# Performance work log

Hardware: AMD Instinct MI355X
Metric: run time of the kernel (lower is better)

## Reference

```python
import jax, jax.numpy as jnp
import numpy as np

N_NODES = 10000
N_EDGES = 640000
D = 128
N_GRAPHS = 16
N_CLASSES = 10


def setup_inputs() -> dict:
    key = jax.random.key(0)
    ks = jax.random.split(key, 12)
    x = jax.random.normal(ks[0], (N_NODES, D), dtype=jnp.float32)
    edge_index = jax.random.randint(ks[1], (2, N_EDGES), 0, N_NODES, dtype=jnp.int64)
    batch_ids = jnp.sort(jax.random.randint(ks[2], (N_NODES,), 0, N_GRAPHS, dtype=jnp.int64))
    s = 1.0 / np.sqrt(D)
    W_in = jax.random.normal(ks[3], (D, D), dtype=jnp.float32) * s
    W_self = jax.random.normal(ks[4], (D, D), dtype=jnp.float32) * s
    b = jnp.zeros((D,), dtype=jnp.float32)
    W_e1 = jax.random.normal(ks[5], (2 * D, D), dtype=jnp.float32) * (1.0 / np.sqrt(2 * D))
    b_e1 = jnp.zeros((D,), dtype=jnp.float32)
    W_e2 = jax.random.normal(ks[6], (D, 1), dtype=jnp.float32) * s
    b_e2 = jnp.zeros((1,), dtype=jnp.float32)
    W_cls = jax.random.normal(ks[7], (D, N_CLASSES), dtype=jnp.float32) * s
    b_cls = jnp.zeros((N_CLASSES,), dtype=jnp.float32)
    return {"x": x, "edge_index": edge_index, "batch_ids": batch_ids,
            "W_in": W_in, "W_self": W_self, "b": b,
            "W_e1": W_e1, "b_e1": b_e1, "W_e2": W_e2, "b_e2": b_e2,
            "W_cls": W_cls, "b_cls": b_cls}


def reference(x, edge_index, batch_ids, W_in, W_self, b, W_e1, b_e1, W_e2, b_e2, W_cls, b_cls):
    src, dst = edge_index[0], edge_index[1]
    # --- gnn(data) -> (z_node, z_graph) : GCN-style message passing ---
    h = x @ W_in                                  # [N, D]
    agg = jax.ops.segment_sum(h[src], dst, num_segments=N_NODES)  # [N, D]
    z_node = jax.nn.relu(agg + x @ W_self + b)    # [N, D]
    # mean pool per graph -> z_graph [B, D]
    sums = jax.ops.segment_sum(z_node, batch_ids, num_segments=N_GRAPHS)
    counts = jax.ops.segment_sum(jnp.ones((N_NODES,), dtype=z_node.dtype), batch_ids, num_segments=N_GRAPHS)
    z_graph = sums / jnp.maximum(counts, 1.0)[:, None]
    # --- edge predictor: gather, concat, MLP ---
    edge_features = jnp.concatenate([z_node[src], z_node[dst]], axis=1)  # [E, 2D]
    pred_edge = jax.nn.relu(edge_features @ W_e1 + b_e1) @ W_e2 + b_e2   # [E, 1]
    # --- classifier ---
    pred_class = z_graph @ W_cls + b_cls          # [B, n_classes]
    return (pred_edge, pred_class)
```

## Files before the change

kernel.cpp:

```cpp
#include <hip/hip_runtime.h>

#define N_NODES   10000
#define N_EDGES   640000
#define DIM       128
#define N_GRAPHS  16
#define N_CLASSES 10

typedef unsigned int uint;
typedef unsigned short ushort;

__device__ __forceinline__ float bf2f(uint lo16) {
    return __uint_as_float(lo16 << 16);
}
__device__ __forceinline__ ushort f2bf(float f) {
    uint u = __float_as_uint(f);
    u += 0x7fffu + ((u >> 16) & 1u);
    return (ushort)(u >> 16);
}

__global__ __launch_bounds__(256) void conv_bf16(
    const float* __restrict__ x, uint* __restrict__ xb)
{
    const int idx = blockIdx.x * 256 + threadIdx.x;
    const float4 v = ((const float4*)x)[idx];
    uint lo = (uint)f2bf(v.x) | ((uint)f2bf(v.y) << 16);
    uint hi = (uint)f2bf(v.z) | ((uint)f2bf(v.w) << 16);
    ((uint2*)xb)[idx] = make_uint2(lo, hi);
}

__global__ __launch_bounds__(256) void hist_dst(
    const int* __restrict__ dst, int* __restrict__ cnt)
{
    const int base = (blockIdx.x * 256 + threadIdx.x) * 4;
    const int d0 = dst[base + 0];
    const int d1 = dst[base + 1];
    const int d2 = dst[base + 2];
    const int d3 = dst[base + 3];
    atomicAdd(&cnt[d0], 1);
    atomicAdd(&cnt[d1], 1);
    atomicAdd(&cnt[d2], 1);
    atomicAdd(&cnt[d3], 1);
}

__global__ __launch_bounds__(256) void count_nodes(
    const int* __restrict__ bid, float* __restrict__ gcnt)
{
    __shared__ int h[N_GRAPHS];
    const int t = threadIdx.x;
    if (t < N_GRAPHS) h[t] = 0;
    __syncthreads();
    for (int n = t; n < N_NODES; n += 256) atomicAdd(&h[bid[n]], 1);
    __syncthreads();
    if (t < N_GRAPHS) gcnt[t] = (float)h[t];
}

__global__ __launch_bounds__(1024) void scan_k(
    const int* __restrict__ cnt, int* __restrict__ cursor)
{
    __shared__ int s[1024];
    const int t = threadIdx.x;
    int local[10];
    int sum = 0;
    if (t < 1000) {
        for (int j = 0; j < 10; ++j) { local[j] = sum; sum += cnt[t * 10 + j]; }
    }
    s[t] = (t < 1000) ? sum : 0;
    __syncthreads();
    for (int st = 1; st < 1024; st <<= 1) {
        int v = (t >= st) ? s[t - st] : 0;
        __syncthreads();
        s[t] += v;
        __syncthreads();
    }
    if (t < 1000) {
        const int off = (t == 0) ? 0 : s[t - 1];
        for (int j = 0; j < 10; ++j) cursor[t * 10 + j] = off + local[j];
    }
}

__global__ __launch_bounds__(256) void fill_csr(
    const int* __restrict__ src, const int* __restrict__ dst,
    int* __restrict__ cursor, uint2* __restrict__ pairs)
{
    const int base = (blockIdx.x * 256 + threadIdx.x) * 4;
    const int d0 = dst[base + 0];
    const int d1 = dst[base + 1];
    const int d2 = dst[base + 2];
    const int d3 = dst[base + 3];
    const int s0 = src[base + 0];
    const int s1 = src[base + 1];
    const int s2 = src[base + 2];
    const int s3 = src[base + 3];
    const int p0 = atomicAdd(&cursor[d0], 1);
    const int p1 = atomicAdd(&cursor[d1], 1);
    const int p2 = atomicAdd(&cursor[d2], 1);
    const int p3 = atomicAdd(&cursor[d3], 1);
    pairs[p0] = make_uint2((uint)s0, (uint)(base + 0));
    pairs[p1] = make_uint2((uint)s1, (uint)(base + 1));
    pairs[p2] = make_uint2((uint)s2, (uint)(base + 2));
    pairs[p3] = make_uint2((uint)s3, (uint)(base + 3));
}

__global__ __launch_bounds__(256) void gather_xb(
    const uint* __restrict__ xb,
    const int* __restrict__ cnt, const int* __restrict__ cursor,
    const uint2* __restrict__ pairs,
    float* __restrict__ XAGG)
{
    const int n    = blockIdx.x * 4 + (threadIdx.x >> 6);
    const int lane = threadIdx.x & 63;
    const int end  = cursor[n];
    int i = end - cnt[n];

    float a0 = 0.f, b0 = 0.f, a1 = 0.f, b1 = 0.f;
    float a2 = 0.f, b2 = 0.f, a3 = 0.f, b3 = 0.f;

    for (; i + 8 <= end; i += 8) {
        const uint v0 = xb[pairs[i + 0].x * 64 + lane];
        const uint v1 = xb[pairs[i + 1].x * 64 + lane];
        const uint v2 = xb[pairs[i + 2].x * 64 + lane];
        const uint v3 = xb[pairs[i + 3].x * 64 + lane];
        const uint v4 = xb[pairs[i + 4].x * 64 + lane];
        const uint v5 = xb[pairs[i + 5].x * 64 + lane];
        const uint v6 = xb[pairs[i + 6].x * 64 + lane];
        const uint v7 = xb[pairs[i + 7].x * 64 + lane];
        a0 += bf2f(v0 & 0xffffu); b0 += bf2f(v0 >> 16);
        a1 += bf2f(v1 & 0xffffu); b1 += bf2f(v1 >> 16);
        a2 += bf2f(v2 & 0xffffu); b2 += bf2f(v2 >> 16);
        a3 += bf2f(v3 & 0xffffu); b3 += bf2f(v3 >> 16);
        a0 += bf2f(v4 & 0xffffu); b0 += bf2f(v4 >> 16);
        a1 += bf2f(v5 & 0xffffu); b1 += bf2f(v5 >> 16);
        a2 += bf2f(v6 & 0xffffu); b2 += bf2f(v6 >> 16);
        a3 += bf2f(v7 & 0xffffu); b3 += bf2f(v7 >> 16);
    }
    for (; i < end; ++i) {
        const uint v = xb[pairs[i].x * 64 + lane];
        a0 += bf2f(v & 0xffffu); b0 += bf2f(v >> 16);
    }
    float2 s;
    s.x = (a0 + a1) + (a2 + a3);
    s.y = (b0 + b1) + (b2 + b3);
    *(float2*)&XAGG[n * DIM + lane * 2] = s;
}

#define ZROWS 8
__global__ __launch_bounds__(256) void gemm_zu(
    const float* __restrict__ XAGG_in, const float* __restrict__ x,
    const float* __restrict__ W_in, const float* __restrict__ W_self,
    const float* __restrict__ b, const int* __restrict__ bid,
    const float* __restrict__ W_e1, const float* __restrict__ b_e1,
    float* __restrict__ gsum, ushort* __restrict__ U12)
{
    __shared__ float sa[ZROWS * DIM];
    __shared__ float sb[ZROWS * DIM];
    __shared__ int sbid[ZROWS];
    const int base = blockIdx.x * ZROWS;
    const int t = threadIdx.x;
    {
        const float4* ga = (const float4*)(XAGG_in + base * DIM);
        const float4* gb = (const float4*)(x + base * DIM);
        float4* la = (float4*)sa;
        float4* lb = (float4*)sb;
        for (int i = t; i < ZROWS * DIM / 4; i += 256) { la[i] = ga[i]; lb[i] = gb[i]; }
        if (t < ZROWS) sbid[t] = bid[base + t];
    }
    __syncthreads();

    const int half = t >> 7, c = t & 127;

    {
        const float* __restrict__ W = half ? W_self : W_in;
        const float4* A4 = (const float4*)(half ? sb : sa);
        float acc[ZROWS];
#pragma unroll
        for (int r = 0; r < ZROWS; ++r) acc[r] = 0.f;
        for (int k4 = 0; k4 < DIM / 4; ++k4) {
            const float w0 = W[(k4 * 4 + 0) * DIM + c];
            const float w1 = W[(k4 * 4 + 1) * DIM + c];
            const float w2 = W[(k4 * 4 + 2) * DIM + c];
            const float w3 = W[(k4 * 4 + 3) * DIM + c];
#pragma unroll
            for (int r = 0; r < ZROWS; ++r) {
                const float4 xv = A4[r * (DIM / 4) + k4];
                acc[r] = fmaf(xv.x, w0, acc[r]);
                acc[r] = fmaf(xv.y, w1, acc[r]);
                acc[r] = fmaf(xv.z, w2, acc[r]);
                acc[r] = fmaf(xv.w, w3, acc[r]);
            }
        }
        __syncthreads();
        if (half) {
#pragma unroll
            for (int r = 0; r < ZROWS; ++r) sb[r * DIM + c] = acc[r];
        }
        __syncthreads();
        if (!half) {
            const float bv = b[c];
            float run = 0.f;
            int cur = sbid[0];
#pragma unroll
            for (int r = 0; r < ZROWS; ++r) {
                const float z = fmaxf(acc[r] + sb[r * DIM + c] + bv, 0.f);
                sa[r * DIM + c] = z;
                const int g = sbid[r];
                if (g != cur) { unsafeAtomicAdd(&gsum[cur * DIM + c], run); run = 0.f; cur = g; }
                run += z;
            }
            unsafeAtomicAdd(&gsum[cur * DIM + c], run);
        }
        __syncthreads();
    }

    {
        const float* __restrict__ W = W_e1 + half * 128 * DIM;
        const float4* Z4 = (const float4*)sa;
        float acc[ZROWS];
#pragma unroll
        for (int r = 0; r < ZROWS; ++r) acc[r] = 0.f;
        for (int k4 = 0; k4 < DIM / 4; ++k4) {
            const float w0 = W[(k4 * 4 + 0) * DIM + c];
            const float w1 = W[(k4 * 4 + 1) * DIM + c];
            const float w2 = W[(k4 * 4 + 2) * DIM + c];
            const float w3 = W[(k4 * 4 + 3) * DIM + c];
#pragma unroll
            for (int r = 0; r < ZROWS; ++r) {
                const float4 xv = Z4[r * (DIM / 4) + k4];
                acc[r] = fmaf(xv.x, w0, acc[r]);
                acc[r] = fmaf(xv.y, w1, acc[r]);
                acc[r] = fmaf(xv.z, w2, acc[r]);
                acc[r] = fmaf(xv.w, w3, acc[r]);
            }
        }
        const float bv = half ? 0.f : b_e1[c];
        for (int r = 0; r < ZROWS; ++r)
            U12[(base + r) * 256 + half * 128 + c] = f2bf(acc[r] + bv);
    }
}

__device__ __forceinline__ void ch2(uint a, uint b, float wl, float wh,
                                    float& accl, float& acch)
{
    const float fl = fmaxf(__uint_as_float(a << 16) + __uint_as_float(b << 16), 0.f);
    const float fh = fmaxf(__uint_as_float(a & 0xffff0000u) + __uint_as_float(b & 0xffff0000u), 0.f);
    accl = fmaf(fl, wl, accl);
    acch = fmaf(fh, wh, acch);
}

__global__ __launch_bounds__(256) void edge_mlp4(
    const ushort* __restrict__ U12,
    const int* __restrict__ cnt, const int* __restrict__ cursor,
    const uint2* __restrict__ pairs,
    const float* __restrict__ W_e2, const float* __restrict__ b_e2,
    float* __restrict__ out)
{
    __shared__ float ws[DIM];
    const int t = threadIdx.x;
    if (t < DIM) ws[t] = W_e2[t];
    __syncthreads();

    const int l16 = t & 15;
    const int grp = t >> 4;
    const int n   = blockIdx.x * 16 + grp;

    const int end = cursor[n];
    int i = end - cnt[n];

    const uint4 u2 = *(const uint4*)(U12 + n * 256 + 128 + l16 * 8);
    const float4 w0 = ((const float4*)ws)[l16 * 2 + 0];
    const float4 w1 = ((const float4*)ws)[l16 * 2 + 1];
    const float be2 = b_e2[0];

    for (; i + 2 <= end; i += 2) {
        const uint2 pa = pairs[i];
        const uint2 pb = pairs[i + 1];
        const uint4 A = *(const uint4*)(U12 + pa.x * 256 + l16 * 8);
        const uint4 B = *(const uint4*)(U12 + pb.x * 256 + l16 * 8);
        float p0 = 0.f, p1 = 0.f, q0 = 0.f, q1 = 0.f;
        ch2(A.x, u2.x, w0.x, w0.y, p0, p1);
        ch2(A.y, u2.y, w0.z, w0.w, p0, p1);
        ch2(A.z, u2.z, w1.x, w1.y, p0, p1);
        ch2(A.w, u2.w, w1.z, w1.w, p0, p1);
        ch2(B.x, u2.x, w0.x, w0.y, q0, q1);
        ch2(B.y, u2.y, w0.z, w0.w, q0, q1);
        ch2(B.z, u2.z, w1.x, w1.y, q0, q1);
        ch2(B.w, u2.w, w1.z, w1.w, q0, q1);
        float p = p0 + p1;
        float q = q0 + q1;
#pragma unroll
        for (int off = 8; off >= 1; off >>= 1) {
            p += __shfl_xor(p, off);
            q += __shfl_xor(q, off);
        }
        if (l16 == 0) { out[pa.y] = p + be2; out[pb.y] = q + be2; }
    }
    if (i < end) {
        const uint2 pa = pairs[i];
        const uint4 A = *(const uint4*)(U12 + pa.x * 256 + l16 * 8);
        float p0 = 0.f, p1 = 0.f;
        ch2(A.x, u2.x, w0.x, w0.y, p0, p1);
        ch2(A.y, u2.y, w0.z, w0.w, p0, p1);
        ch2(A.z, u2.z, w1.x, w1.y, p0, p1);
        ch2(A.w, u2.w, w1.z, w1.w, p0, p1);
        float p = p0 + p1;
#pragma unroll
        for (int off = 8; off >= 1; off >>= 1)
            p += __shfl_xor(p, off);
        if (l16 == 0) out[pa.y] = p + be2;
    }
}

__global__ __launch_bounds__(256) void classify(
    const float* __restrict__ gsum, const float* __restrict__ gcnt,
    const float* __restrict__ W_cls, const float* __restrict__ b_cls,
    float* __restrict__ out)
{
    const int t = threadIdx.x;
    if (t >= N_GRAPHS * N_CLASSES) return;
    const int g = t / N_CLASSES;
    const int c = t % N_CLASSES;
    const float inv = 1.0f / fmaxf(gcnt[g], 1.0f);
    float acc = 0.f;
    for (int k = 0; k < DIM; ++k)
        acc += gsum[g * DIM + k] * W_cls[k * N_CLASSES + c];
    out[g * N_CLASSES + c] = acc * inv + b_cls[c];
}

extern "C" void kernel_launch(void* const* d_in, const int* in_sizes, int n_in,
                              void* d_out, int out_size, void* d_ws, size_t ws_size,
                              hipStream_t stream)
{
    const float* x      = (const float*)d_in[0];
    const int*   eidx   = (const int*)  d_in[1];
    const int*   bid    = (const int*)  d_in[2];
    const float* W_in   = (const float*)d_in[3];
    const float* W_self = (const float*)d_in[4];
    const float* b      = (const float*)d_in[5];
    const float* W_e1   = (const float*)d_in[6];
    const float* b_e1   = (const float*)d_in[7];
    const float* W_e2   = (const float*)d_in[8];
    const float* b_e2   = (const float*)d_in[9];
    const float* W_cls  = (const float*)d_in[10];
    const float* b_cls  = (const float*)d_in[11];
    float* out = (float*)d_out;

    char* ws = (char*)d_ws;
    int*    cnt    = (int*)   (ws);
    float*  gsum   = (float*) (ws + 40960);
    float*  gcnt   = (float*) (ws + 49152);
    int*    cursor = (int*)   (ws + 65536);
    uint2*  pairs  = (uint2*) (ws + 131072);
    float*  XAGG   = (float*) (ws + 131072 + 5120000);
    ushort* U12    = (ushort*)(ws + 131072 + 10240000);
    uint*   xb     = (uint*)  (ws + 131072 + 15360000);

    const int* src = eidx;
    const int* dst = eidx + N_EDGES;

    hipMemsetAsync(d_ws, 0, 65536, stream);

    conv_bf16  <<<(N_NODES * DIM / 4) / 256, 256, 0, stream>>>(x, xb);
    hist_dst   <<<N_EDGES / 1024, 256, 0, stream>>>(dst, cnt);
    count_nodes<<<1, 256, 0, stream>>>(bid, gcnt);
    scan_k     <<<1, 1024, 0, stream>>>(cnt, cursor);
    fill_csr   <<<N_EDGES / 1024, 256, 0, stream>>>(src, dst, cursor, pairs);
    gather_xb  <<<N_NODES / 4, 256, 0, stream>>>(xb, cnt, cursor, pairs, XAGG);
    gemm_zu    <<<N_NODES / ZROWS, 256, 0, stream>>>(XAGG, x, W_in, W_self, b, bid,
                                                     W_e1, b_e1, gsum, U12);
    edge_mlp4  <<<N_NODES / 16, 256, 0, stream>>>(U12, cnt, cursor, pairs, W_e2, b_e2, out);
    classify   <<<1, 256, 0, stream>>>(gsum, gcnt, W_cls, b_cls, out + N_EDGES);
}
```

Baseline: 282.4 us.

## Process edge MLP per edge in original order and shrink CSR to source-only

The edge predictor no longer walks the dst-sorted CSR. It now assigns two edges per 16-lane group in original edge order and gathers both the source and destination U12 rows directly, writing outputs with coalesced float2 stores. Because edge ids are no longer needed, the CSR array shrinks from (src, edge id) pairs to src only, which halves fill_csr writes and gather_xb index reads. In exchange, the edge kernel loses reuse of the per-destination U2 row and does one extra random gather per edge, but it gains perfect load balance and coalesced output.

New measurement: 262.1 us. 7.2% less time.

```diff
diff --git a/kernel.cpp b/kernel.cpp
--- a/kernel.cpp
+++ b/kernel.cpp
@@ -80,7 +80,7 @@
 
 __global__ __launch_bounds__(256) void fill_csr(
     const int* __restrict__ src, const int* __restrict__ dst,
-    int* __restrict__ cursor, uint2* __restrict__ pairs)
+    int* __restrict__ cursor, uint* __restrict__ srcs)
 {
     const int base = (blockIdx.x * 256 + threadIdx.x) * 4;
     const int d0 = dst[base + 0];
@@ -95,16 +95,16 @@
     const int p1 = atomicAdd(&cursor[d1], 1);
     const int p2 = atomicAdd(&cursor[d2], 1);
     const int p3 = atomicAdd(&cursor[d3], 1);
-    pairs[p0] = make_uint2((uint)s0, (uint)(base + 0));
-    pairs[p1] = make_uint2((uint)s1, (uint)(base + 1));
-    pairs[p2] = make_uint2((uint)s2, (uint)(base + 2));
-    pairs[p3] = make_uint2((uint)s3, (uint)(base + 3));
+    srcs[p0] = (uint)s0;
+    srcs[p1] = (uint)s1;
+    srcs[p2] = (uint)s2;
+    srcs[p3] = (uint)s3;
 }
 
 __global__ __launch_bounds__(256) void gather_xb(
     const uint* __restrict__ xb,
     const int* __restrict__ cnt, const int* __restrict__ cursor,
-    const uint2* __restrict__ pairs,
+    const uint* __restrict__ srcs,
     float* __restrict__ XAGG)
 {
     const int n    = blockIdx.x * 4 + (threadIdx.x >> 6);
@@ -116,14 +116,14 @@
     float a2 = 0.f, b2 = 0.f, a3 = 0.f, b3 = 0.f;
 
     for (; i + 8 <= end; i += 8) {
-        const uint v0 = xb[pairs[i + 0].x * 64 + lane];
-        const uint v1 = xb[pairs[i + 1].x * 64 + lane];
-        const uint v2 = xb[pairs[i + 2].x * 64 + lane];
-        const uint v3 = xb[pairs[i + 3].x * 64 + lane];
-        const uint v4 = xb[pairs[i + 4].x * 64 + lane];
-        const uint v5 = xb[pairs[i + 5].x * 64 + lane];
-        const uint v6 = xb[pairs[i + 6].x * 64 + lane];
-        const uint v7 = xb[pairs[i + 7].x * 64 + lane];
+        const uint v0 = xb[srcs[i + 0] * 64 + lane];
+        const uint v1 = xb[srcs[i + 1] * 64 + lane];
+        const uint v2 = xb[srcs[i + 2] * 64 + lane];
+        const uint v3 = xb[srcs[i + 3] * 64 + lane];
+        const uint v4 = xb[srcs[i + 4] * 64 + lane];
+        const uint v5 = xb[srcs[i + 5] * 64 + lane];
+        const uint v6 = xb[srcs[i + 6] * 64 + lane];
+        const uint v7 = xb[srcs[i + 7] * 64 + lane];
         a0 += bf2f(v0 & 0xffffu); b0 += bf2f(v0 >> 16);
         a1 += bf2f(v1 & 0xffffu); b1 += bf2f(v1 >> 16);
         a2 += bf2f(v2 & 0xffffu); b2 += bf2f(v2 >> 16);
@@ -134,7 +134,7 @@
         a3 += bf2f(v7 & 0xffffu); b3 += bf2f(v7 >> 16);
     }
     for (; i < end; ++i) {
-        const uint v = xb[pairs[i].x * 64 + lane];
+        const uint v = xb[srcs[i] * 64 + lane];
         a0 += bf2f(v & 0xffffu); b0 += bf2f(v >> 16);
     }
     float2 s;
@@ -246,10 +246,9 @@
     acch = fmaf(fh, wh, acch);
 }
 
-__global__ __launch_bounds__(256) void edge_mlp4(
+__global__ __launch_bounds__(256) void edge_mlp5(
     const ushort* __restrict__ U12,
-    const int* __restrict__ cnt, const int* __restrict__ cursor,
-    const uint2* __restrict__ pairs,
+    const int* __restrict__ src, const int* __restrict__ dst,
     const float* __restrict__ W_e2, const float* __restrict__ b_e2,
     float* __restrict__ out)
 {
@@ -260,52 +259,40 @@
 
     const int l16 = t & 15;
     const int grp = t >> 4;
-    const int n   = blockIdx.x * 16 + grp;
-
-    const int end = cursor[n];
-    int i = end - cnt[n];
-
-    const uint4 u2 = *(const uint4*)(U12 + n * 256 + 128 + l16 * 8);
+    const int e0  = blockIdx.x * 32 + grp * 2;
+    const int e1  = e0 + 1;
+
+    const int s0 = src[e0], d0 = dst[e0];
+    const int s1 = src[e1], d1 = dst[e1];
+
+    const uint4 A0 = *(const uint4*)(U12 + s0 * 256 + l16 * 8);
+    const uint4 B0 = *(const uint4*)(U12 + d0 * 256 + 128 + l16 * 8);
+    const uint4 A1 = *(const uint4*)(U12 + s1 * 256 + l16 * 8);
+    const uint4 B1 = *(const uint4*)(U12 + d1 * 256 + 128 + l16 * 8);
     const float4 w0 = ((const float4*)ws)[l16 * 2 + 0];
     const float4 w1 = ((const float4*)ws)[l16 * 2 + 1];
-    const float be2 = b_e2[0];
-
-    for (; i + 2 <= end; i += 2) {
-        const uint2 pa = pairs[i];
-        const uint2 pb = pairs[i + 1];
-        const uint4 A = *(const uint4*)(U12 + pa.x * 256 + l16 * 8);
-        const uint4 B = *(const uint4*)(U12 + pb.x * 256 + l16 * 8);
-        float p0 = 0.f, p1 = 0.f, q0 = 0.f, q1 = 0.f;
-        ch2(A.x, u2.x, w0.x, w0.y, p0, p1);
-        ch2(A.y, u2.y, w0.z, w0.w, p0, p1);
-        ch2(A.z, u2.z, w1.x, w1.y, p0, p1);
-        ch2(A.w, u2.w, w1.z, w1.w, p0, p1);
-        ch2(B.x, u2.x, w0.x, w0.y, q0, q1);
-        ch2(B.y, u2.y, w0.z, w0.w, q0, q1);
-        ch2(B.z, u2.z, w1.x, w1.y, q0, q1);
-        ch2(B.w, u2.w, w1.z, w1.w, q0, q1);
-        float p = p0 + p1;
-        float q = q0 + q1;
-#pragma unroll
-        for (int off = 8; off >= 1; off >>= 1) {
-            p += __shfl_xor(p, off);
-            q += __shfl_xor(q, off);
-        }
-        if (l16 == 0) { out[pa.y] = p + be2; out[pb.y] = q + be2; }
-    }
-    if (i < end) {
-        const uint2 pa = pairs[i];
-        const uint4 A = *(const uint4*)(U12 + pa.x * 256 + l16 * 8);
-        float p0 = 0.f, p1 = 0.f;
-        ch2(A.x, u2.x, w0.x, w0.y, p0, p1);
-        ch2(A.y, u2.y, w0.z, w0.w, p0, p1);
-        ch2(A.z, u2.z, w1.x, w1.y, p0, p1);
-        ch2(A.w, u2.w, w1.z, w1.w, p0, p1);
-        float p = p0 + p1;
-#pragma unroll
-        for (int off = 8; off >= 1; off >>= 1)
-            p += __shfl_xor(p, off);
-        if (l16 == 0) out[pa.y] = p + be2;
+
+    float p0 = 0.f, p1 = 0.f, q0 = 0.f, q1 = 0.f;
+    ch2(A0.x, B0.x, w0.x, w0.y, p0, p1);
+    ch2(A0.y, B0.y, w0.z, w0.w, p0, p1);
+    ch2(A0.z, B0.z, w1.x, w1.y, p0, p1);
+    ch2(A0.w, B0.w, w1.z, w1.w, p0, p1);
+    ch2(A1.x, B1.x, w0.x, w0.y, q0, q1);
+    ch2(A1.y, B1.y, w0.z, w0.w, q0, q1);
+    ch2(A1.z, B1.z, w1.x, w1.y, q0, q1);
+    ch2(A1.w, B1.w, w1.z, w1.w, q0, q1);
+
+    float p = p0 + p1;
+    float q = q0 + q1;
+#pragma unroll
+    for (int off = 8; off >= 1; off >>= 1) {
+        p += __shfl_xor(p, off);
+        q += __shfl_xor(q, off);
+    }
+
+    if (l16 == 0) {
+        const float be2 = b_e2[0];
+        *(float2*)&out[e0] = make_float2(p + be2, q + be2);
     }
 }
 
@@ -348,10 +335,10 @@
     float*  gsum   = (float*) (ws + 40960);
     float*  gcnt   = (float*) (ws + 49152);
     int*    cursor = (int*)   (ws + 65536);
-    uint2*  pairs  = (uint2*) (ws + 131072);
-    float*  XAGG   = (float*) (ws + 131072 + 5120000);
-    ushort* U12    = (ushort*)(ws + 131072 + 10240000);
-    uint*   xb     = (uint*)  (ws + 131072 + 15360000);
+    uint*   srcs   = (uint*)  (ws + 131072);
+    float*  XAGG   = (float*) (ws + 131072 + 2560000);
+    ushort* U12    = (ushort*)(ws + 131072 + 7680000);
+    uint*   xb     = (uint*)  (ws + 131072 + 12800000);
 
     const int* src = eidx;
     const int* dst = eidx + N_EDGES;
@@ -362,10 +349,10 @@
     hist_dst   <<<N_EDGES / 1024, 256, 0, stream>>>(dst, cnt);
     count_nodes<<<1, 256, 0, stream>>>(bid, gcnt);
     scan_k     <<<1, 1024, 0, stream>>>(cnt, cursor);
-    fill_csr   <<<N_EDGES / 1024, 256, 0, stream>>>(src, dst, cursor, pairs);
-    gather_xb  <<<N_NODES / 4, 256, 0, stream>>>(xb, cnt, cursor, pairs, XAGG);
+    fill_csr   <<<N_EDGES / 1024, 256, 0, stream>>>(src, dst, cursor, srcs);
+    gather_xb  <<<N_NODES / 4, 256, 0, stream>>>(xb, cnt, cursor, srcs, XAGG);
     gemm_zu    <<<N_NODES / ZROWS, 256, 0, stream>>>(XAGG, x, W_in, W_self, b, bid,
                                                      W_e1, b_e1, gsum, U12);
-    edge_mlp4  <<<N_NODES / 16, 256, 0, stream>>>(U12, cnt, cursor, pairs, W_e2, b_e2, out);
+    edge_mlp5  <<<N_EDGES / 32, 256, 0, stream>>>(U12, src, dst, W_e2, b_e2, out);
     classify   <<<1, 256, 0, stream>>>(gsum, gcnt, W_cls, b_cls, out + N_EDGES);
 }
```
